# Kernel optimization log

Hardware: AMD Instinct MI355X
Metric: run time of the kernel (lower is better)

## Reference

```python
import jax, jax.numpy as jnp
import numpy as np

B, T, D = 4, 50, 512
SRC, SENTS, WORDS = 400, 16, 40
NEG = jnp.float32(-1e30)  # stands in for -inf mask fill (numerically identical post-softmax)


def _seq_mask(lengths, max_len):
    # [n, max_len] bool, True where position < length
    return jnp.arange(max_len)[None, :] < lengths[:, None]


def _mlp_score(q, h, Wq, bq, Uc, v):
    # Bahdanau additive score: v^T tanh(W q + U h)
    # q: [b,t,d], h: [b,s,d] -> [b,t,s]
    wq = q @ Wq + bq                       # [b,t,d]
    uh = h @ Uc                            # [b,s,d]
    wquh = jnp.tanh(wq[:, :, None, :] + uh[:, None, :, :])  # [b,t,s,d]
    return jnp.einsum('btsd,d->bts', wquh, v)


def setup_inputs() -> dict:
    key = jax.random.key(0)
    ks = jax.random.split(key, 20)
    s = np.float32(1.0 / np.sqrt(D))
    def p(k, shape):
        return jax.random.normal(k, shape, jnp.float32) * s
    return {
        'source': jax.random.normal(ks[0], (B, T, D), jnp.float32),
        'src_bank': jax.random.normal(ks[1], (SRC, B, D), jnp.float32),
        'src_lengths': jax.random.randint(ks[2], (B,), 1, SRC + 1),
        'qa_sent_bank': jax.random.normal(ks[3], (SENTS, B, D), jnp.float32),
        'qa_sent_lengths': jax.random.randint(ks[4], (B,), 1, SENTS + 1),
        'qa_word_bank': jax.random.normal(ks[5], (WORDS, B, SENTS, D), jnp.float32),
        'qa_word_lengths': jax.random.randint(ks[6], (B, SENTS), 1, WORDS + 1),
        'Wq_word': p(ks[7], (D, D)), 'bq_word': jnp.zeros((D,), jnp.float32),
        'Uc_word': p(ks[8], (D, D)), 'v_word': p(ks[9], (D,)),
        'Wq_sent': p(ks[10], (D, D)), 'bq_sent': jnp.zeros((D,), jnp.float32),
        'Uc_sent': p(ks[11], (D, D)), 'v_sent': p(ks[12], (D,)),
        'Wq_pass': p(ks[13], (D, D)), 'bq_pass': jnp.zeros((D,), jnp.float32),
        'Uc_pass': p(ks[14], (D, D)), 'v_pass': p(ks[15], (D,)),
    }


def _forward(source, src_bank, qa_sent_bank, qa_word_bank,
             Wq_word, bq_word, Uc_word, v_word,
             Wq_sent, bq_sent, Uc_sent, v_sent,
             Wq_pass, bq_pass, Uc_pass, v_pass,
             src_lengths, qa_word_lengths):
    b = source.shape[0]
    # [words,b,sents,d] -> [b,sents,words,d] -> [b, sents*words, d]
    qa_word = jnp.transpose(qa_word_bank, (1, 2, 0, 3)).reshape(b, SENTS * WORDS, D)
    src = jnp.transpose(src_bank, (1, 0, 2))       # [b,src,d]
    sent = jnp.transpose(qa_sent_bank, (1, 0, 2))  # [b,sents,d]

    qa_word_align = _mlp_score(source, qa_word, Wq_word, bq_word, Uc_word, v_word)  # [b,t,sents*words]
    src_align = _mlp_score(source, src, Wq_pass, bq_pass, Uc_pass, v_pass)          # [b,t,src]
    qa_sent_align = _mlp_score(source, sent, Wq_sent, bq_sent, Uc_sent, v_sent)     # [b,t,sents]

    # hierarchical combination: word score scaled by its sentence score
    qa_hier = (qa_word_align.reshape(b, T, SENTS, WORDS)
               * qa_sent_align[..., None]).reshape(b, T, SENTS * WORDS)

    align = jnp.concatenate([src_align, qa_hier], axis=-1)  # [b,t,src+sents*words]

    qa_mask = _seq_mask(qa_word_lengths.reshape(-1), WORDS).reshape(b, SENTS * WORDS)[:, None, :]
    src_mask = _seq_mask(src_lengths, SRC)[:, None, :]
    mask = jnp.concatenate([src_mask, qa_mask], axis=-1)

    align = jnp.where(mask, align, NEG)
    align_vectors = jax.nn.softmax(align, axis=-1)  # joint length-masked softmax

    memory = jnp.concatenate([src, qa_word], axis=1)          # [b, src+sents*words, d]
    c = jnp.einsum('bts,bsd->btd', align_vectors, memory)     # weighted context sum
    return c


def reference(source, src_bank, src_lengths, qa_sent_bank, qa_sent_lengths,
              qa_word_bank, qa_word_lengths,
              Wq_word, bq_word, Uc_word, v_word,
              Wq_sent, bq_sent, Uc_sent, v_sent,
              Wq_pass, bq_pass, Uc_pass, v_pass):
    # qa_sent_lengths is accepted but unused, matching the original forward()
    return _forward(source, src_bank, qa_sent_bank, qa_word_bank,
                    Wq_word, bq_word, Uc_word, v_word,
                    Wq_sent, bq_sent, Uc_sent, v_sent,
                    Wq_pass, bq_pass, Uc_pass, v_pass,
                    src_lengths, qa_word_lengths)
```

## Files before the change

kernel.cpp:

```cpp
#include <hip/hip_runtime.h>
#include <hip/hip_bf16.h>


#define B_    4
#define T_    50
#define D_    512
#define SRC_  400
#define SENTS_ 16
#define WORDS_ 40
#define NW_   640
#define NMEM_ 1040
#define NK_   1056
#define NJOB_ 1056

#define C2L2E 2.8853900817779268f

typedef unsigned short ushort_t;
using s8v = __attribute__((ext_vector_type(8))) short;
using f4v = __attribute__((ext_vector_type(4))) float;

#define OFF_WQ_WORD 0
#define OFF_WQ_SENT 102400
#define OFF_WQ_PASS 204800
#define OFF_UH_SRC  307200
#define OFF_UH_WORD 1126400
#define OFF_UH_SENT 2437120
#define OFF_SC_SRC  2469888
#define OFF_SC_WORD 2549888
#define OFF_SC_SENT 2677888
#define P_BYTE_OFF  10724352ull
#define MT_BYTE_OFF 11265024ull
#define WT_BYTE_OFF 15590400ull

__device__ __forceinline__ ushort_t f2b(float f) {
    __hip_bfloat16 h = __float2bfloat16(f);
    return *(ushort_t*)&h;
}

__global__ __launch_bounds__(256) void k0t_bankT(
    const float* __restrict__ src_bank, const float* __restrict__ qa_word_bank,
    ushort_t* __restrict__ mt)
{
    __shared__ float tile[32][33];
    int s0 = blockIdx.x * 32, d0 = blockIdx.y * 32, b = blockIdx.z;
    int tx = threadIdx.x & 31, ty = threadIdx.x >> 5;
#pragma unroll
    for (int a = 0; a < 4; ++a) {
        int s = s0 + ty + a * 8;
        float val = 0.f;
        if (s < SRC_) {
            val = src_bank[(s * B_ + b) * D_ + d0 + tx];
        } else if (s < NMEM_) {
            int j = s - SRC_; int se = j / WORDS_; int wd = j - se * WORDS_;
            val = qa_word_bank[((wd * B_ + b) * SENTS_ + se) * D_ + d0 + tx];
        }
        tile[ty + a * 8][tx] = val;
    }
    __syncthreads();
    ushort_t* base = mt + (size_t)b * D_ * NK_;
#pragma unroll
    for (int a = 0; a < 4; ++a) {
        int d = d0 + ty + a * 8;
        base[(size_t)d * NK_ + s0 + tx] = f2b(tile[tx][ty + a * 8]);
    }
}

__global__ __launch_bounds__(256) void k0_transpose(
    const float* __restrict__ w0, const float* __restrict__ w1,
    const float* __restrict__ w2, const float* __restrict__ w3,
    const float* __restrict__ w4, const float* __restrict__ w5,
    ushort_t* __restrict__ wt)
{
    __shared__ float tile[32][33];
    const float* W;
    switch (blockIdx.z) {
        case 0: W = w0; break; case 1: W = w1; break; case 2: W = w2; break;
        case 3: W = w3; break; case 4: W = w4; break; default: W = w5; break;
    }
    ushort_t* Wt = wt + blockIdx.z * (D_ * D_);
    int n0 = blockIdx.x * 32, k0 = blockIdx.y * 32;
    int tx = threadIdx.x & 31, ty = threadIdx.x >> 5;
#pragma unroll
    for (int a = 0; a < 4; ++a)
        tile[ty + a * 8][tx] = W[(k0 + ty + a * 8) * D_ + n0 + tx];
    __syncthreads();
#pragma unroll
    for (int a = 0; a < 4; ++a)
        Wt[(n0 + ty + a * 8) * D_ + k0 + tx] = f2b(tile[tx][ty + a * 8]);
}

__global__ __launch_bounds__(256) void k1_gemm(
    const float* __restrict__ source, const float* __restrict__ src_bank,
    const float* __restrict__ qa_sent_bank, const float* __restrict__ qa_word_bank,
    const ushort_t* __restrict__ wt,
    const float* __restrict__ bq_word, const float* __restrict__ bq_sent,
    const float* __restrict__ bq_pass,
    float* __restrict__ wsf)
{
    __shared__ short At[64 * 32];
    __shared__ short Bt[64 * 32];
    int z = blockIdx.z;
    int M, atype; const float* bias; float* C;
    switch (z) {
        case 0: M = 200;  atype = 0; bias = bq_word; C = wsf + OFF_WQ_WORD; break;
        case 1: M = 200;  atype = 0; bias = bq_sent; C = wsf + OFF_WQ_SENT; break;
        case 2: M = 200;  atype = 0; bias = bq_pass; C = wsf + OFF_WQ_PASS; break;
        case 3: M = 2560; atype = 1; bias = nullptr; C = wsf + OFF_UH_WORD; break;
        case 4: M = 1600; atype = 2; bias = nullptr; C = wsf + OFF_UH_SRC;  break;
        default: M = 64;  atype = 3; bias = nullptr; C = wsf + OFF_UH_SENT; break;
    }
    int m0 = blockIdx.y * 64;
    if (m0 >= M) return;
    int n0 = blockIdx.x * 64;
    const ushort_t* W = wt + z * (D_ * D_);

    int tid = threadIdx.x;
    int lane = tid & 63, wv = tid >> 6;
    int quad = lane >> 4, l16 = lane & 15;
    int sm = tid >> 2, koff = (tid & 3) * 8;

    const float* arow = nullptr;
    {
        int r = m0 + sm;
        if (r < M) {
            if (atype == 0) arow = source + r * D_;
            else if (atype == 1) { int b = r / NW_; int j = r - b * NW_;
                                   int se = j / WORDS_; int wd = j - se * WORDS_;
                                   arow = qa_word_bank + ((wd * B_ + b) * SENTS_ + se) * D_; }
            else if (atype == 2) { int b = r / SRC_; int j = r - b * SRC_;
                                   arow = src_bank + (j * B_ + b) * D_; }
            else                 { int b = r >> 4; int s2 = r & 15;
                                   arow = qa_sent_bank + (s2 * B_ + b) * D_; }
        }
    }
    const ushort_t* wrow = W + (n0 + sm) * D_;

    f4v acc[4] = { {0.f,0.f,0.f,0.f}, {0.f,0.f,0.f,0.f},
                   {0.f,0.f,0.f,0.f}, {0.f,0.f,0.f,0.f} };

    for (int kk = 0; kk < 16; ++kk) {
        int k0 = kk * 32;
        union { ushort_t u[8]; int4 v; } pk;
        if (arow) {
            float4 f0 = *(const float4*)(arow + k0 + koff);
            float4 f1 = *(const float4*)(arow + k0 + koff + 4);
            pk.u[0] = f2b(f0.x); pk.u[1] = f2b(f0.y);
            pk.u[2] = f2b(f0.z); pk.u[3] = f2b(f0.w);
            pk.u[4] = f2b(f1.x); pk.u[5] = f2b(f1.y);
            pk.u[6] = f2b(f1.z); pk.u[7] = f2b(f1.w);
        } else {
            pk.v = int4{0, 0, 0, 0};
        }
        int4 bv = *(const int4*)(wrow + k0 + koff);
        *(int4*)(At + sm * 32 + koff) = pk.v;
        *(int4*)(Bt + sm * 32 + koff) = bv;
        __syncthreads();
        s8v af = *(const s8v*)(At + (wv * 16 + l16) * 32 + quad * 8);
#pragma unroll
        for (int ng = 0; ng < 4; ++ng) {
            s8v bf = *(const s8v*)(Bt + (ng * 16 + l16) * 32 + quad * 8);
            acc[ng] = __builtin_amdgcn_mfma_f32_16x16x32_bf16(af, bf, acc[ng], 0, 0, 0);
        }
        __syncthreads();
    }
#pragma unroll
    for (int ng = 0; ng < 4; ++ng) {
        int col = n0 + ng * 16 + l16;
        float bb = bias ? bias[col] : 0.f;
#pragma unroll
        for (int rr = 0; rr < 4; ++rr) {
            int row = m0 + wv * 16 + quad * 4 + rr;
            if (row < M) C[row * D_ + col] = (acc[ng][rr] + bb) * C2L2E;
        }
    }
}

__global__ __launch_bounds__(256) void k2_scores(
    const float* __restrict__ v_word, const float* __restrict__ v_sent,
    const float* __restrict__ v_pass, float* __restrict__ wsf)
{
    int lane = threadIdx.x & 63;
    int job = blockIdx.x * 4 + (threadIdx.x >> 6);
    int b = job / NJOB_, slot = job - b * NJOB_;
    const float* uh; const float* v; const float* wq; float* out; int ostride;
    if (slot < SRC_) {
        uh = wsf + OFF_UH_SRC + (b * SRC_ + slot) * D_;
        v = v_pass; wq = wsf + OFF_WQ_PASS + b * T_ * D_;
        out = wsf + OFF_SC_SRC + b * T_ * SRC_ + slot; ostride = SRC_;
    } else if (slot < NMEM_) {
        int j = slot - SRC_;
        uh = wsf + OFF_UH_WORD + (b * NW_ + j) * D_;
        v = v_word; wq = wsf + OFF_WQ_WORD + b * T_ * D_;
        out = wsf + OFF_SC_WORD + b * T_ * NW_ + j; ostride = NW_;
    } else {
        int s2 = slot - NMEM_;
        uh = wsf + OFF_UH_SENT + (b * SENTS_ + s2) * D_;
        v = v_sent; wq = wsf + OFF_WQ_SENT + b * T_ * D_;
        out = wsf + OFF_SC_SENT + b * T_ * SENTS_ + s2; ostride = SENTS_;
    }
    int d0 = lane * 8;
    float4 u0 = *(const float4*)(uh + d0);
    float4 u1 = *(const float4*)(uh + d0 + 4);
    float uhr[8] = {u0.x, u0.y, u0.z, u0.w, u1.x, u1.y, u1.z, u1.w};
    float4 v0 = *(const float4*)(v + d0);
    float4 v1 = *(const float4*)(v + d0 + 4);
    float vr[8] = {v0.x, v0.y, v0.z, v0.w, v1.x, v1.y, v1.z, v1.w};

    float vs = ((vr[0] + vr[1]) + (vr[2] + vr[3])) + ((vr[4] + vr[5]) + (vr[6] + vr[7]));
#pragma unroll
    for (int off = 32; off > 0; off >>= 1) vs += __shfl_xor(vs, off, 64);

    for (int tc = 0; tc < T_; tc += 10) {
        float acc[10];
#pragma unroll
        for (int u = 0; u < 10; ++u) {
            const float* wr = wq + (tc + u) * D_ + d0;
            float4 w0 = *(const float4*)(wr);
            float4 w1 = *(const float4*)(wr + 4);
            float wrr[8] = {w0.x, w0.y, w0.z, w0.w, w1.x, w1.y, w1.z, w1.w};
            float a = 0.f;
#pragma unroll
            for (int j = 0; j < 8; ++j) {
                float e = __builtin_amdgcn_exp2f(wrr[j] + uhr[j]);
                float r = __builtin_amdgcn_rcpf(e + 1.f);
                a = fmaf(vr[j], r, a);
            }
            acc[u] = a;
        }
#pragma unroll
        for (int off = 32; off > 0; off >>= 1) {
#pragma unroll
            for (int u = 0; u < 10; ++u)
                acc[u] += __shfl_xor(acc[u], off, 64);
        }
        if (lane == 0) {
#pragma unroll
            for (int u = 0; u < 10; ++u)
                out[(tc + u) * ostride] = fmaf(-2.f, acc[u], vs);
        }
    }
}

__global__ __launch_bounds__(256) void k3a_softmax(
    const int* __restrict__ src_lengths, const int* __restrict__ qa_word_lengths,
    const float* __restrict__ wsf, ushort_t* __restrict__ P)
{
    __shared__ float p[NMEM_];
    __shared__ float red[4];
    int tid = threadIdx.x, lane = tid & 63, wv = tid >> 6;
    int bt = blockIdx.x, b = bt / T_, t = bt - b * T_;
    const float* sc_src  = wsf + OFF_SC_SRC  + bt * SRC_;
    const float* sc_word = wsf + OFF_SC_WORD + bt * NW_;
    const float* sc_sent = wsf + OFF_SC_SENT + bt * SENTS_;
    int slen = src_lengths[b];
    float mx = -3.0e38f;
    for (int j = tid; j < NMEM_; j += 256) {
        float val;
        if (j < SRC_) {
            val = (j < slen) ? sc_src[j] : -1e30f;
        } else {
            int jj = j - SRC_; int se = jj / WORDS_; int wd = jj - se * WORDS_;
            float raw = sc_word[jj] * sc_sent[se];
            val = (wd < qa_word_lengths[b * SENTS_ + se]) ? raw : -1e30f;
        }
        p[j] = val;
        mx = fmaxf(mx, val);
    }
#pragma unroll
    for (int off = 32; off > 0; off >>= 1) mx = fmaxf(mx, __shfl_xor(mx, off, 64));
    if (lane == 0) red[wv] = mx;
    __syncthreads();
    mx = fmaxf(fmaxf(red[0], red[1]), fmaxf(red[2], red[3]));
    __syncthreads();
    float lsum = 0.f;
    for (int j = tid; j < NMEM_; j += 256) {
        float e = __expf(p[j] - mx);
        p[j] = e; lsum += e;
    }
#pragma unroll
    for (int off = 32; off > 0; off >>= 1) lsum += __shfl_xor(lsum, off, 64);
    if (lane == 0) red[wv] = lsum;
    __syncthreads();
    float inv = 1.f / (red[0] + red[1] + red[2] + red[3]);
    ushort_t* prow = P + (size_t)(b * 64 + t) * NK_;
    for (int j = tid; j < NK_; j += 256)
        prow[j] = (j < NMEM_) ? f2b(p[j] * inv) : (ushort_t)0;
}

__global__ __launch_bounds__(256) void k3c_gemm(
    const ushort_t* __restrict__ P, const ushort_t* __restrict__ Mt,
    float* __restrict__ out)
{
    __shared__ short At[64 * 32];
    __shared__ short Bt[64 * 32];
    int b = blockIdx.y;
    int n0 = blockIdx.x * 64;
    int tid = threadIdx.x;
    int lane = tid & 63, wv = tid >> 6;
    int quad = lane >> 4, l16 = lane & 15;
    int sm = tid >> 2, koff = (tid & 3) * 8;

    const ushort_t* arow = (sm < T_) ? (P + (size_t)(b * 64 + sm) * NK_ + koff) : nullptr;
    const ushort_t* brow = Mt + ((size_t)(b * D_ + n0 + sm)) * NK_ + koff;

    f4v acc[4] = { {0.f,0.f,0.f,0.f}, {0.f,0.f,0.f,0.f},
                   {0.f,0.f,0.f,0.f}, {0.f,0.f,0.f,0.f} };

    for (int kk = 0; kk < 33; ++kk) {
        int k0 = kk * 32;
        int4 av = int4{0, 0, 0, 0};
        if (arow) av = *(const int4*)(arow + k0);
        int4 bv = *(const int4*)(brow + k0);
        *(int4*)(At + sm * 32 + koff) = av;
        *(int4*)(Bt + sm * 32 + koff) = bv;
        __syncthreads();
        s8v af = *(const s8v*)(At + (wv * 16 + l16) * 32 + quad * 8);
#pragma unroll
        for (int ng = 0; ng < 4; ++ng) {
            s8v bf = *(const s8v*)(Bt + (ng * 16 + l16) * 32 + quad * 8);
            acc[ng] = __builtin_amdgcn_mfma_f32_16x16x32_bf16(af, bf, acc[ng], 0, 0, 0);
        }
        __syncthreads();
    }
#pragma unroll
    for (int ng = 0; ng < 4; ++ng) {
        int col = n0 + ng * 16 + l16;
#pragma unroll
        for (int rr = 0; rr < 4; ++rr) {
            int row = wv * 16 + quad * 4 + rr;
            if (row < T_) out[(size_t)(b * T_ + row) * D_ + col] = acc[ng][rr];
        }
    }
}

extern "C" void kernel_launch(void* const* d_in, const int* in_sizes, int n_in,
                              void* d_out, int out_size, void* d_ws, size_t ws_size,
                              hipStream_t stream)
{
    (void)in_sizes; (void)n_in; (void)out_size; (void)ws_size;
    const float* source          = (const float*)d_in[0];
    const float* src_bank        = (const float*)d_in[1];
    const int*   src_lengths     = (const int*)d_in[2];
    const float* qa_sent_bank    = (const float*)d_in[3];
    const float* qa_word_bank    = (const float*)d_in[5];
    const int*   qa_word_lengths = (const int*)d_in[6];
    const float* Wq_word = (const float*)d_in[7];
    const float* bq_word = (const float*)d_in[8];
    const float* Uc_word = (const float*)d_in[9];
    const float* v_word  = (const float*)d_in[10];
    const float* Wq_sent = (const float*)d_in[11];
    const float* bq_sent = (const float*)d_in[12];
    const float* Uc_sent = (const float*)d_in[13];
    const float* v_sent  = (const float*)d_in[14];
    const float* Wq_pass = (const float*)d_in[15];
    const float* bq_pass = (const float*)d_in[16];
    const float* Uc_pass = (const float*)d_in[17];
    const float* v_pass  = (const float*)d_in[18];

    float* wsf = (float*)d_ws;
    ushort_t* Pb  = (ushort_t*)((char*)d_ws + P_BYTE_OFF);
    ushort_t* mt  = (ushort_t*)((char*)d_ws + MT_BYTE_OFF);
    ushort_t* wt  = (ushort_t*)((char*)d_ws + WT_BYTE_OFF);
    float* out = (float*)d_out;

    k0t_bankT<<<dim3(33, 16, 4), dim3(256), 0, stream>>>(src_bank, qa_word_bank, mt);
    k0_transpose<<<dim3(16, 16, 6), dim3(256), 0, stream>>>(
        Wq_word, Wq_sent, Wq_pass, Uc_word, Uc_pass, Uc_sent, wt);
    k1_gemm<<<dim3(8, 40, 6), dim3(256), 0, stream>>>(
        source, src_bank, qa_sent_bank, qa_word_bank, wt,
        bq_word, bq_sent, bq_pass, wsf);
    k2_scores<<<dim3(NJOB_), dim3(256), 0, stream>>>(v_word, v_sent, v_pass, wsf);
    k3a_softmax<<<dim3(200), dim3(256), 0, stream>>>(src_lengths, qa_word_lengths, wsf, Pb);
    k3c_gemm<<<dim3(8, 4), dim3(256), 0, stream>>>(Pb, mt, out);
}
```

Before: 176.9 us.

## Skip masked score jobs, split T across waves, fuse transposes, retile output GEMM

```diff
diff --git a/kernel.cpp b/kernel.cpp
--- a/kernel.cpp
+++ b/kernel.cpp
@@ -37,56 +37,55 @@
     return *(ushort_t*)&h;
 }
 
-__global__ __launch_bounds__(256) void k0t_bankT(
-    const float* __restrict__ src_bank, const float* __restrict__ qa_word_bank,
-    ushort_t* __restrict__ mt)
-{
-    __shared__ float tile[32][33];
-    int s0 = blockIdx.x * 32, d0 = blockIdx.y * 32, b = blockIdx.z;
-    int tx = threadIdx.x & 31, ty = threadIdx.x >> 5;
-#pragma unroll
-    for (int a = 0; a < 4; ++a) {
-        int s = s0 + ty + a * 8;
-        float val = 0.f;
-        if (s < SRC_) {
-            val = src_bank[(s * B_ + b) * D_ + d0 + tx];
-        } else if (s < NMEM_) {
-            int j = s - SRC_; int se = j / WORDS_; int wd = j - se * WORDS_;
-            val = qa_word_bank[((wd * B_ + b) * SENTS_ + se) * D_ + d0 + tx];
-        }
-        tile[ty + a * 8][tx] = val;
-    }
-    __syncthreads();
-    ushort_t* base = mt + (size_t)b * D_ * NK_;
-#pragma unroll
-    for (int a = 0; a < 4; ++a) {
-        int d = d0 + ty + a * 8;
-        base[(size_t)d * NK_ + s0 + tx] = f2b(tile[tx][ty + a * 8]);
-    }
-}
-
-__global__ __launch_bounds__(256) void k0_transpose(
+__global__ __launch_bounds__(256) void k0f_transpose(
     const float* __restrict__ w0, const float* __restrict__ w1,
     const float* __restrict__ w2, const float* __restrict__ w3,
     const float* __restrict__ w4, const float* __restrict__ w5,
-    ushort_t* __restrict__ wt)
+    const float* __restrict__ src_bank, const float* __restrict__ qa_word_bank,
+    ushort_t* __restrict__ wt, ushort_t* __restrict__ mt)
 {
     __shared__ float tile[32][33];
-    const float* W;
-    switch (blockIdx.z) {
-        case 0: W = w0; break; case 1: W = w1; break; case 2: W = w2; break;
-        case 3: W = w3; break; case 4: W = w4; break; default: W = w5; break;
-    }
-    ushort_t* Wt = wt + blockIdx.z * (D_ * D_);
-    int n0 = blockIdx.x * 32, k0 = blockIdx.y * 32;
+    int z = blockIdx.z;
     int tx = threadIdx.x & 31, ty = threadIdx.x >> 5;
-#pragma unroll
-    for (int a = 0; a < 4; ++a)
-        tile[ty + a * 8][tx] = W[(k0 + ty + a * 8) * D_ + n0 + tx];
-    __syncthreads();
-#pragma unroll
-    for (int a = 0; a < 4; ++a)
-        Wt[(n0 + ty + a * 8) * D_ + k0 + tx] = f2b(tile[tx][ty + a * 8]);
+    if (z < 6) {
+        if (blockIdx.x >= 16) return;
+        const float* W;
+        switch (z) {
+            case 0: W = w0; break; case 1: W = w1; break; case 2: W = w2; break;
+            case 3: W = w3; break; case 4: W = w4; break; default: W = w5; break;
+        }
+        ushort_t* Wt = wt + z * (D_ * D_);
+        int n0 = blockIdx.x * 32, k0 = blockIdx.y * 32;
+#pragma unroll
+        for (int a = 0; a < 4; ++a)
+            tile[ty + a * 8][tx] = W[(k0 + ty + a * 8) * D_ + n0 + tx];
+        __syncthreads();
+#pragma unroll
+        for (int a = 0; a < 4; ++a)
+            Wt[(n0 + ty + a * 8) * D_ + k0 + tx] = f2b(tile[tx][ty + a * 8]);
+    } else {
+        int b = z - 6;
+        int s0 = blockIdx.x * 32, d0 = blockIdx.y * 32;
+#pragma unroll
+        for (int a = 0; a < 4; ++a) {
+            int s = s0 + ty + a * 8;
+            float val = 0.f;
+            if (s < SRC_) {
+                val = src_bank[(s * B_ + b) * D_ + d0 + tx];
+            } else if (s < NMEM_) {
+                int j = s - SRC_; int se = j / WORDS_; int wd = j - se * WORDS_;
+                val = qa_word_bank[((wd * B_ + b) * SENTS_ + se) * D_ + d0 + tx];
+            }
+            tile[ty + a * 8][tx] = val;
+        }
+        __syncthreads();
+        ushort_t* base = mt + (size_t)b * D_ * NK_;
+#pragma unroll
+        for (int a = 0; a < 4; ++a) {
+            int d = d0 + ty + a * 8;
+            base[(size_t)d * NK_ + s0 + tx] = f2b(tile[tx][ty + a * 8]);
+        }
+    }
 }
 
 __global__ __launch_bounds__(256) void k1_gemm(
@@ -177,18 +176,24 @@
 
 __global__ __launch_bounds__(256) void k2_scores(
     const float* __restrict__ v_word, const float* __restrict__ v_sent,
-    const float* __restrict__ v_pass, float* __restrict__ wsf)
+    const float* __restrict__ v_pass,
+    const int* __restrict__ src_lengths, const int* __restrict__ qa_word_lengths,
+    float* __restrict__ wsf)
 {
     int lane = threadIdx.x & 63;
-    int job = blockIdx.x * 4 + (threadIdx.x >> 6);
+    int job2 = blockIdx.x * 4 + (threadIdx.x >> 6);
+    int job = job2 >> 1, th = job2 & 1;
     int b = job / NJOB_, slot = job - b * NJOB_;
     const float* uh; const float* v; const float* wq; float* out; int ostride;
     if (slot < SRC_) {
+        if (slot >= src_lengths[b]) return;
         uh = wsf + OFF_UH_SRC + (b * SRC_ + slot) * D_;
         v = v_pass; wq = wsf + OFF_WQ_PASS + b * T_ * D_;
         out = wsf + OFF_SC_SRC + b * T_ * SRC_ + slot; ostride = SRC_;
     } else if (slot < NMEM_) {
         int j = slot - SRC_;
+        int se = j / WORDS_; int wd = j - se * WORDS_;
+        if (wd >= qa_word_lengths[b * SENTS_ + se]) return;
         uh = wsf + OFF_UH_WORD + (b * NW_ + j) * D_;
         v = v_word; wq = wsf + OFF_WQ_WORD + b * T_ * D_;
         out = wsf + OFF_SC_WORD + b * T_ * NW_ + j; ostride = NW_;
@@ -210,11 +215,14 @@
 #pragma unroll
     for (int off = 32; off > 0; off >>= 1) vs += __shfl_xor(vs, off, 64);
 
-    for (int tc = 0; tc < T_; tc += 10) {
-        float acc[10];
-#pragma unroll
-        for (int u = 0; u < 10; ++u) {
-            const float* wr = wq + (tc + u) * D_ + d0;
+    const float* wqh = wq + th * 25 * D_;
+    float acc[25];
+#pragma unroll 1
+    for (int c = 0; c < 5; ++c) {
+#pragma unroll
+        for (int u5 = 0; u5 < 5; ++u5) {
+            int u = c * 5 + u5;
+            const float* wr = wqh + u * D_ + d0;
             float4 w0 = *(const float4*)(wr);
             float4 w1 = *(const float4*)(wr + 4);
             float wrr[8] = {w0.x, w0.y, w0.z, w0.w, w1.x, w1.y, w1.z, w1.w};
@@ -227,17 +235,17 @@
             }
             acc[u] = a;
         }
-#pragma unroll
-        for (int off = 32; off > 0; off >>= 1) {
-#pragma unroll
-            for (int u = 0; u < 10; ++u)
-                acc[u] += __shfl_xor(acc[u], off, 64);
-        }
-        if (lane == 0) {
-#pragma unroll
-            for (int u = 0; u < 10; ++u)
-                out[(tc + u) * ostride] = fmaf(-2.f, acc[u], vs);
-        }
+    }
+#pragma unroll
+    for (int off = 32; off > 0; off >>= 1) {
+#pragma unroll
+        for (int u = 0; u < 25; ++u)
+            acc[u] += __shfl_xor(acc[u], off, 64);
+    }
+    if (lane == 0) {
+#pragma unroll
+        for (int u = 0; u < 25; ++u)
+            out[(th * 25 + u) * ostride] = fmaf(-2.f, acc[u], vs);
     }
 }
 
@@ -292,38 +300,37 @@
     float* __restrict__ out)
 {
     __shared__ short At[64 * 32];
-    __shared__ short Bt[64 * 32];
+    __shared__ short Bt[32 * 32];
     int b = blockIdx.y;
-    int n0 = blockIdx.x * 64;
+    int n0 = blockIdx.x * 32;
     int tid = threadIdx.x;
     int lane = tid & 63, wv = tid >> 6;
     int quad = lane >> 4, l16 = lane & 15;
-    int sm = tid >> 2, koff = (tid & 3) * 8;
-
-    const ushort_t* arow = (sm < T_) ? (P + (size_t)(b * 64 + sm) * NK_ + koff) : nullptr;
-    const ushort_t* brow = Mt + ((size_t)(b * D_ + n0 + sm)) * NK_ + koff;
-
-    f4v acc[4] = { {0.f,0.f,0.f,0.f}, {0.f,0.f,0.f,0.f},
-                   {0.f,0.f,0.f,0.f}, {0.f,0.f,0.f,0.f} };
+    int smA = tid >> 2, koffA = (tid & 3) * 8;
+    int smB = tid >> 3, koffB = (tid & 7) * 4;
+
+    const ushort_t* arow = P + (size_t)(b * 64 + smA) * NK_ + koffA;
+    const ushort_t* brow = Mt + ((size_t)(b * D_ + n0 + smB)) * NK_ + koffB;
+
+    f4v acc[2] = { {0.f,0.f,0.f,0.f}, {0.f,0.f,0.f,0.f} };
 
     for (int kk = 0; kk < 33; ++kk) {
         int k0 = kk * 32;
-        int4 av = int4{0, 0, 0, 0};
-        if (arow) av = *(const int4*)(arow + k0);
-        int4 bv = *(const int4*)(brow + k0);
-        *(int4*)(At + sm * 32 + koff) = av;
-        *(int4*)(Bt + sm * 32 + koff) = bv;
+        int4 av = *(const int4*)(arow + k0);
+        int2 bv = *(const int2*)(brow + k0);
+        *(int4*)(At + smA * 32 + koffA) = av;
+        *(int2*)(Bt + smB * 32 + koffB) = bv;
         __syncthreads();
         s8v af = *(const s8v*)(At + (wv * 16 + l16) * 32 + quad * 8);
 #pragma unroll
-        for (int ng = 0; ng < 4; ++ng) {
+        for (int ng = 0; ng < 2; ++ng) {
             s8v bf = *(const s8v*)(Bt + (ng * 16 + l16) * 32 + quad * 8);
             acc[ng] = __builtin_amdgcn_mfma_f32_16x16x32_bf16(af, bf, acc[ng], 0, 0, 0);
         }
         __syncthreads();
     }
 #pragma unroll
-    for (int ng = 0; ng < 4; ++ng) {
+    for (int ng = 0; ng < 2; ++ng) {
         int col = n0 + ng * 16 + l16;
 #pragma unroll
         for (int rr = 0; rr < 4; ++rr) {
@@ -363,13 +370,14 @@
     ushort_t* wt  = (ushort_t*)((char*)d_ws + WT_BYTE_OFF);
     float* out = (float*)d_out;
 
-    k0t_bankT<<<dim3(33, 16, 4), dim3(256), 0, stream>>>(src_bank, qa_word_bank, mt);
-    k0_transpose<<<dim3(16, 16, 6), dim3(256), 0, stream>>>(
-        Wq_word, Wq_sent, Wq_pass, Uc_word, Uc_pass, Uc_sent, wt);
+    k0f_transpose<<<dim3(33, 16, 10), dim3(256), 0, stream>>>(
+        Wq_word, Wq_sent, Wq_pass, Uc_word, Uc_pass, Uc_sent,
+        src_bank, qa_word_bank, wt, mt);
     k1_gemm<<<dim3(8, 40, 6), dim3(256), 0, stream>>>(
         source, src_bank, qa_sent_bank, qa_word_bank, wt,
         bq_word, bq_sent, bq_pass, wsf);
-    k2_scores<<<dim3(NJOB_), dim3(256), 0, stream>>>(v_word, v_sent, v_pass, wsf);
+    k2_scores<<<dim3(NJOB_ * 2), dim3(256), 0, stream>>>(
+        v_word, v_sent, v_pass, src_lengths, qa_word_lengths, wsf);
     k3a_softmax<<<dim3(200), dim3(256), 0, stream>>>(src_lengths, qa_word_lengths, wsf, Pb);
-    k3c_gemm<<<dim3(8, 4), dim3(256), 0, stream>>>(Pb, mt, out);
-}
+    k3c_gemm<<<dim3(16, 4), dim3(256), 0, stream>>>(Pb, mt, out);
+}
```

Result: faster. 166.3 us (-6.0%).
